# Kernel tuning notes

Measured on AMD Instinct MI355X. Metric: run time of the kernel, lower is better.

The kernel has to match this reference:

```python
import jax, jax.numpy as jnp
import numpy as np

B, CIN, COUT, H, W, KS, PAD = 8, 64, 128, 32, 32, 3, 1
OH, OW = H, W  # stride 1, pad 1, dilation 1 -> same spatial size
QMIN, QMAX = -128, 127


def setup_inputs() -> dict:
    key = jax.random.key(0)
    k1, k2, k3 = jax.random.split(key, 3)
    x = jax.random.normal(k1, (B, CIN, H, W), jnp.float32)
    weight = jax.random.normal(k2, (COUT, CIN, KS, KS), jnp.float32) * 0.05
    bias = jax.random.normal(k3, (COUT,), jnp.float32) * 0.01
    # exact int8 product LUT: lut[a+128, b+128] = a*b (the 'approximate multiplier' table)
    q = jnp.arange(QMIN, QMAX + 1, dtype=jnp.int32)  # [256]
    lut = q[:, None] * q[None, :]                     # [256,256] int32
    # gradient LUT: d(a*b)/da = b, d(a*b)/db = a
    gradient_lut = jnp.stack([
        jnp.broadcast_to(q[None, :], (256, 256)),
        jnp.broadcast_to(q[:, None], (256, 256)),
    ]).astype(jnp.float32)                            # [2,256,256]
    T_feature = jnp.ones((1,), jnp.float32)
    T_weight = jnp.ones((1,), jnp.float32)
    return {"x": x, "weight": weight, "bias": bias, "lut": lut,
            "gradient_lut": gradient_lut, "T_feature": T_feature, "T_weight": T_weight}


def _quantize(v, T):
    scale = 127.0 / T
    return jnp.clip(jnp.round(v * scale), QMIN, QMAX).astype(jnp.int32)


def _lut_conv(xq, wq, lut):
    """LUT-based int8 conv. xq [B,CIN,H,W] int32 in [-128,127], wq [COUT,CIN,KS,KS]."""
    xp = jnp.pad(xq, ((0, 0), (0, 0), (PAD, PAD), (PAD, PAD)))
    # im2col: 9 structurally-distinct kernel offsets (fixed small loop)
    patches = jnp.stack([xp[:, :, i:i + OH, j:j + OW]
                         for i in range(KS) for j in range(KS)], axis=2)  # [B,CIN,9,OH,OW]
    K = CIN * KS * KS
    cols = patches.transpose(0, 3, 4, 1, 2).reshape(B * OH * OW, K)  # [P,K]
    wf = wq.reshape(COUT, K)                                         # [COUT,K]
    lut_flat = lut.reshape(-1)

    def step(acc, xs):
        xk, wk = xs  # xk [P], wk [COUT]
        idx = (xk[:, None] + 128) * 256 + (wk[None, :] + 128)  # [P,COUT]
        return acc + lut_flat[idx], None

    acc0 = jnp.zeros((B * OH * OW, COUT), jnp.int32)
    acc, _ = jax.lax.scan(step, acc0, (cols.T, wf.T))  # scan over K patch elems
    return acc.reshape(B, OH, OW, COUT).transpose(0, 3, 1, 2)  # [B,COUT,OH,OW]


def reference(x, weight, bias, lut, gradient_lut, T_feature, T_weight):
    # EMA threshold update (update_T_func), detached scalars in the original
    Tf = 0.95 * T_feature[0] + 0.05 * jnp.max(jnp.abs(x))
    Tw = 0.95 * T_weight[0] + 0.05 * jnp.max(jnp.abs(weight))
    xq = _quantize(x, Tf)
    wq = _quantize(weight, Tw)
    acc = _lut_conv(xq, wq, lut).astype(jnp.float32)
    out = acc * ((Tf / 127.0) * (Tw / 127.0)) + bias[None, :, None, None]
    return out
```

## Files before the change

### kernel.cpp

```cpp
#include <hip/hip_runtime.h>
#include <cstdint>

#define BATCH 8
#define CIN 64
#define COUT 128
#define HH 32
#define WW 32

typedef int v4i __attribute__((ext_vector_type(4)));
typedef float v4f __attribute__((ext_vector_type(4)));

#define WS_TW 1
#define WS_PX 16
#define WFRAG_OFF 4096

#define TPITCH 18

__device__ __forceinline__ unsigned quantb(float v, float scale) {
    float q = rintf(v * scale);
    q = fminf(fmaxf(q, -128.0f), 127.0f);
    return ((unsigned)(int)q) & 255u;
}

__global__ __launch_bounds__(256) void prep(const float* __restrict__ x,
                                            const float* __restrict__ w,
                                            const float* __restrict__ Tw_in,
                                            float* __restrict__ ws_f32,
                                            uint8_t* __restrict__ wfrag) {
    int blk = blockIdx.x;
    int t = threadIdx.x;
    int lane = t & 63;
    int wave = t >> 6;
    __shared__ float sm[4];

    if (blk >= 18) {
        const float4* p = (const float4*)x;
        int xb = blk - 18;
        int base = xb * 1024 + t;
        float m = 0.0f;
        #pragma unroll
        for (int k = 0; k < 4; ++k) {
            float4 v = p[base + k * 256];
            m = fmaxf(m, fmaxf(fmaxf(fabsf(v.x), fabsf(v.y)), fmaxf(fabsf(v.z), fabsf(v.w))));
        }
        #pragma unroll
        for (int off = 32; off > 0; off >>= 1)
            m = fmaxf(m, __shfl_xor(m, off, 64));
        if (lane == 0) sm[wave] = m;
        __syncthreads();
        if (t == 0)
            ws_f32[WS_PX + xb] = fmaxf(fmaxf(sm[0], sm[1]), fmaxf(sm[2], sm[3]));
    } else {
        const float4* w4 = (const float4*)w;
        float m0 = 0.0f, m1 = 0.0f, m2 = 0.0f, m3 = 0.0f;
        #pragma unroll
        for (int i = 0; i < 72; i += 4) {
            float4 a = w4[t + (i + 0) * 256];
            float4 bv = w4[t + (i + 1) * 256];
            float4 c = w4[t + (i + 2) * 256];
            float4 d = w4[t + (i + 3) * 256];
            m0 = fmaxf(m0, fmaxf(fmaxf(fabsf(a.x), fabsf(a.y)), fmaxf(fabsf(a.z), fabsf(a.w))));
            m1 = fmaxf(m1, fmaxf(fmaxf(fabsf(bv.x), fabsf(bv.y)), fmaxf(fabsf(bv.z), fabsf(bv.w))));
            m2 = fmaxf(m2, fmaxf(fmaxf(fabsf(c.x), fabsf(c.y)), fmaxf(fabsf(c.z), fabsf(c.w))));
            m3 = fmaxf(m3, fmaxf(fmaxf(fabsf(d.x), fabsf(d.y)), fmaxf(fabsf(d.z), fabsf(d.w))));
        }
        float m = fmaxf(fmaxf(m0, m1), fmaxf(m2, m3));
        #pragma unroll
        for (int off = 32; off > 0; off >>= 1)
            m = fmaxf(m, __shfl_xor(m, off, 64));
        if (lane == 0) sm[wave] = m;
        __syncthreads();
        float Mw = fmaxf(fmaxf(sm[0], sm[1]), fmaxf(sm[2], sm[3]));
        float Tw = 0.95f * Tw_in[0] + 0.05f * Mw;
        if (blk == 0 && t == 0) ws_f32[WS_TW] = Tw;
        float scale = 127.0f / Tw;

        int wb = blk;
        #pragma unroll
        for (int k = 0; k < 4; ++k) {
            int d = wb * 1024 + k * 256 + t;
            int idx4 = d * 4;
            int j0 = idx4 & 15;
            int ln = (idx4 >> 4) & 63;
            int f  = idx4 >> 10;
            int g = f & 7;
            int tap = f >> 3;
            int kh = tap / 3, kw = tap - kh * 3;
            int co = g * 16 + (ln & 15);
            int ci0 = (ln >> 4) * 16 + j0;
            unsigned pack = 0;
            #pragma unroll
            for (int c = 0; c < 4; ++c) {
                float v = w[((co * CIN + ci0 + c) * 3 + kh) * 3 + kw];
                pack |= quantb(v, scale) << (8 * c);
            }
            ((unsigned*)wfrag)[d] = pack;
        }
    }
}

__global__ __launch_bounds__(256, 2) void conv_fused(const float* __restrict__ x,
                                                     const uint8_t* __restrict__ wfrag,
                                                     const float* __restrict__ bias,
                                                     const float* __restrict__ Tf_in,
                                                     const float* __restrict__ ws_f32,
                                                     float* __restrict__ out) {
    int blk = blockIdx.x;
    int t = threadIdx.x;
    int lane = t & 63;
    int wave = t >> 6;
    int nb = blk & 1;
    int mb = blk >> 1;
    int b = mb >> 5;
    int oh = mb & 31;

    __shared__ unsigned tile[3 * 34 * TPITCH];

    float p0 = ws_f32[WS_PX + lane];
    float p1 = ws_f32[WS_PX + 64 + lane];
    float Tw = ws_f32[WS_TW];

    if (t < 96) {
        int rr = t >> 5;
        int rest = t & 31;
        int side = rest >> 4;
        int kk = rest & 15;
        tile[(rr * 34 + side * 33) * TPITCH + kk] = 0u;
    }
    if (oh == 0 || oh == 31) {
        int rbad = (oh == 0) ? 0 : 2;
        #pragma unroll
        for (int k = 0; k < 3; ++k) {
            int i = t + k * 256;
            if (i < 544) {
                int px = i >> 4, kk = i & 15;
                tile[(rbad * 34 + px) * TPITCH + kk] = 0u;
            }
        }
    }

    float mx = fmaxf(p0, p1);
    #pragma unroll
    for (int off = 32; off > 0; off >>= 1)
        mx = fmaxf(mx, __shfl_xor(mx, off, 64));
    float Tf = 0.95f * Tf_in[0] + 0.05f * mx;
    float scale = 127.0f / Tf;

    const float4* x4 = (const float4*)x;
    #pragma unroll
    for (int k = 0; k < 2; ++k) {
        int j = t + k * 256;
        if (j < 384) {
            int r = j >> 7;
            int rem = j & 127;
            int wq = rem >> 4;
            int g4 = rem & 15;
            int ih = oh - 1 + r;
            if (ih >= 0 && ih < HH) {
                int xb = (b * CIN + g4 * 4) * 256 + ih * 8 + wq;
                float4 v0 = x4[xb];
                float4 v1 = x4[xb + 256];
                float4 v2 = x4[xb + 512];
                float4 v3 = x4[xb + 768];
                unsigned P0 = quantb(v0.x, scale) | (quantb(v0.y, scale) << 8) |
                              (quantb(v0.z, scale) << 16) | (quantb(v0.w, scale) << 24);
                unsigned P1 = quantb(v1.x, scale) | (quantb(v1.y, scale) << 8) |
                              (quantb(v1.z, scale) << 16) | (quantb(v1.w, scale) << 24);
                unsigned P2 = quantb(v2.x, scale) | (quantb(v2.y, scale) << 8) |
                              (quantb(v2.z, scale) << 16) | (quantb(v2.w, scale) << 24);
                unsigned P3 = quantb(v3.x, scale) | (quantb(v3.y, scale) << 8) |
                              (quantb(v3.z, scale) << 16) | (quantb(v3.w, scale) << 24);
                unsigned Q0 = __builtin_amdgcn_perm(P1, P0, 0x05040100u);
                unsigned Q1 = __builtin_amdgcn_perm(P1, P0, 0x07060302u);
                unsigned Q2 = __builtin_amdgcn_perm(P3, P2, 0x05040100u);
                unsigned Q3 = __builtin_amdgcn_perm(P3, P2, 0x07060302u);
                unsigned D0 = __builtin_amdgcn_perm(Q2, Q0, 0x06040200u);
                unsigned D1 = __builtin_amdgcn_perm(Q2, Q0, 0x07050301u);
                unsigned D2 = __builtin_amdgcn_perm(Q3, Q1, 0x06040200u);
                unsigned D3 = __builtin_amdgcn_perm(Q3, Q1, 0x07050301u);
                int base = (r * 34 + wq * 4 + 1) * TPITCH + g4;
                tile[base]              = D0;
                tile[base + TPITCH]     = D1;
                tile[base + 2 * TPITCH] = D2;
                tile[base + 3 * TPITCH] = D3;
            }
        }
    }
    __syncthreads();

    int mt = wave & 1;
    int nh2 = wave >> 1;
    int row = lane & 15;
    int quad = lane >> 4;
    int px0 = mt * 16 + row;

    v4i acc[2];
    acc[0] = (v4i){0, 0, 0, 0};
    acc[1] = (v4i){0, 0, 0, 0};

    const int2* tl2 = (const int2*)tile;

    #pragma unroll
    for (int tp = 0; tp < 9; ++tp) {
        const int kh = tp / 3, kw = tp % 3;
        int d = ((kh * 34) + px0 + kw) * TPITCH + quad * 4;
        int2 lo = tl2[(d >> 1)];
        int2 hi = tl2[(d >> 1) + 1];
        v4i afrag = (v4i){lo.x, lo.y, hi.x, hi.y};
        #pragma unroll
        for (int nt = 0; nt < 2; ++nt) {
            int g = nb * 4 + nh2 * 2 + nt;
            v4i bfrag = *(const v4i*)(wfrag + (((tp * 8 + g) * 64) + lane) * 16);
            acc[nt] = __builtin_amdgcn_mfma_i32_16x16x64_i8(afrag, bfrag, acc[nt], 0, 0, 0);
        }
    }

    float s = (Tf / 127.0f) * (Tw / 127.0f);
    int ow0 = mt * 16 + quad * 4;
    #pragma unroll
    for (int nt = 0; nt < 2; ++nt) {
        int g = nb * 4 + nh2 * 2 + nt;
        int co = g * 16 + row;
        float bb = bias[co];
        v4f o;
        o.x = (float)acc[nt][0] * s + bb;
        o.y = (float)acc[nt][1] * s + bb;
        o.z = (float)acc[nt][2] * s + bb;
        o.w = (float)acc[nt][3] * s + bb;
        __builtin_nontemporal_store(o, (v4f*)(out + (((b * COUT + co) * HH + oh) * WW) + ow0));
    }
}

extern "C" void kernel_launch(void* const* d_in, const int* in_sizes, int n_in,
                              void* d_out, int out_size, void* d_ws, size_t ws_size,
                              hipStream_t stream) {
    const float* x         = (const float*)d_in[0];
    const float* weight    = (const float*)d_in[1];
    const float* bias      = (const float*)d_in[2];
    const float* T_feature = (const float*)d_in[5];
    const float* T_weight  = (const float*)d_in[6];

    float*   ws_f32 = (float*)d_ws;
    uint8_t* wfrag  = (uint8_t*)d_ws + WFRAG_OFF;

    prep<<<146, 256, 0, stream>>>(x, weight, T_weight, ws_f32, wfrag);
    conv_fused<<<512, 256, 0, stream>>>(x, wfrag, bias, T_feature, ws_f32,
                                        (float*)d_out);
}
```

Baseline: 78.51 us.

## Fuse weight quantization into conv kernel, parallelize weight max reduction across blocks

The prep kernel no longer quantizes and repacks the weights into a global fragment buffer. It now only computes per-block partial abs-max values for x and w, with the weight reduction spread over 24 blocks instead of repeated in 18. Each conv block reduces both partials itself, derives Tw, and quantizes its own 64-channel half of the weights straight into a 36KB LDS fragment buffer. This removes the serial per-block full-weight scan and one global round-trip, but every one of the 512 blocks now redoes weight loading and quantization, and the extra LDS may lower occupancy.

After: 78.95 us. About the same (+0.6%).

```diff
diff --git a/kernel.cpp b/kernel.cpp
--- a/kernel.cpp
+++ b/kernel.cpp
@@ -10,9 +10,8 @@
 typedef int v4i __attribute__((ext_vector_type(4)));
 typedef float v4f __attribute__((ext_vector_type(4)));
 
-#define WS_TW 1
 #define WS_PX 16
-#define WFRAG_OFF 4096
+#define WS_PW 160
 
 #define TPITCH 18
 
@@ -22,87 +21,50 @@
     return ((unsigned)(int)q) & 255u;
 }
 
-__global__ __launch_bounds__(256) void prep(const float* __restrict__ x,
-                                            const float* __restrict__ w,
-                                            const float* __restrict__ Tw_in,
-                                            float* __restrict__ ws_f32,
-                                            uint8_t* __restrict__ wfrag) {
+__global__ __launch_bounds__(256) void partials(const float* __restrict__ x,
+                                                const float* __restrict__ w,
+                                                float* __restrict__ ws_f32) {
     int blk = blockIdx.x;
     int t = threadIdx.x;
     int lane = t & 63;
     int wave = t >> 6;
     __shared__ float sm[4];
 
-    if (blk >= 18) {
+    float m = 0.0f;
+    if (blk < 128) {
         const float4* p = (const float4*)x;
-        int xb = blk - 18;
-        int base = xb * 1024 + t;
-        float m = 0.0f;
+        int base = blk * 1024 + t;
         #pragma unroll
         for (int k = 0; k < 4; ++k) {
             float4 v = p[base + k * 256];
             m = fmaxf(m, fmaxf(fmaxf(fabsf(v.x), fabsf(v.y)), fmaxf(fabsf(v.z), fabsf(v.w))));
         }
-        #pragma unroll
-        for (int off = 32; off > 0; off >>= 1)
-            m = fmaxf(m, __shfl_xor(m, off, 64));
-        if (lane == 0) sm[wave] = m;
-        __syncthreads();
-        if (t == 0)
-            ws_f32[WS_PX + xb] = fmaxf(fmaxf(sm[0], sm[1]), fmaxf(sm[2], sm[3]));
     } else {
-        const float4* w4 = (const float4*)w;
-        float m0 = 0.0f, m1 = 0.0f, m2 = 0.0f, m3 = 0.0f;
-        #pragma unroll
-        for (int i = 0; i < 72; i += 4) {
-            float4 a = w4[t + (i + 0) * 256];
-            float4 bv = w4[t + (i + 1) * 256];
-            float4 c = w4[t + (i + 2) * 256];
-            float4 d = w4[t + (i + 3) * 256];
-            m0 = fmaxf(m0, fmaxf(fmaxf(fabsf(a.x), fabsf(a.y)), fmaxf(fabsf(a.z), fabsf(a.w))));
-            m1 = fmaxf(m1, fmaxf(fmaxf(fabsf(bv.x), fabsf(bv.y)), fmaxf(fabsf(bv.z), fabsf(bv.w))));
-            m2 = fmaxf(m2, fmaxf(fmaxf(fabsf(c.x), fabsf(c.y)), fmaxf(fabsf(c.z), fabsf(c.w))));
-            m3 = fmaxf(m3, fmaxf(fmaxf(fabsf(d.x), fabsf(d.y)), fmaxf(fabsf(d.z), fabsf(d.w))));
-        }
-        float m = fmaxf(fmaxf(m0, m1), fmaxf(m2, m3));
-        #pragma unroll
-        for (int off = 32; off > 0; off >>= 1)
-            m = fmaxf(m, __shfl_xor(m, off, 64));
-        if (lane == 0) sm[wave] = m;
-        __syncthreads();
-        float Mw = fmaxf(fmaxf(sm[0], sm[1]), fmaxf(sm[2], sm[3]));
-        float Tw = 0.95f * Tw_in[0] + 0.05f * Mw;
-        if (blk == 0 && t == 0) ws_f32[WS_TW] = Tw;
-        float scale = 127.0f / Tw;
-
-        int wb = blk;
-        #pragma unroll
-        for (int k = 0; k < 4; ++k) {
-            int d = wb * 1024 + k * 256 + t;
-            int idx4 = d * 4;
-            int j0 = idx4 & 15;
-            int ln = (idx4 >> 4) & 63;
-            int f  = idx4 >> 10;
-            int g = f & 7;
-            int tap = f >> 3;
-            int kh = tap / 3, kw = tap - kh * 3;
-            int co = g * 16 + (ln & 15);
-            int ci0 = (ln >> 4) * 16 + j0;
-            unsigned pack = 0;
-            #pragma unroll
-            for (int c = 0; c < 4; ++c) {
-                float v = w[((co * CIN + ci0 + c) * 3 + kh) * 3 + kw];
-                pack |= quantb(v, scale) << (8 * c);
-            }
-            ((unsigned*)wfrag)[d] = pack;
-        }
+        const float4* p = (const float4*)w;
+        int base = (blk - 128) * 768 + t;
+        #pragma unroll
+        for (int k = 0; k < 3; ++k) {
+            float4 v = p[base + k * 256];
+            m = fmaxf(m, fmaxf(fmaxf(fabsf(v.x), fabsf(v.y)), fmaxf(fabsf(v.z), fabsf(v.w))));
+        }
+    }
+    #pragma unroll
+    for (int off = 32; off > 0; off >>= 1)
+        m = fmaxf(m, __shfl_xor(m, off, 64));
+    if (lane == 0) sm[wave] = m;
+    __syncthreads();
+    if (t == 0) {
+        float r = fmaxf(fmaxf(sm[0], sm[1]), fmaxf(sm[2], sm[3]));
+        if (blk < 128) ws_f32[WS_PX + blk] = r;
+        else           ws_f32[WS_PW + (blk - 128)] = r;
     }
 }
 
 __global__ __launch_bounds__(256, 2) void conv_fused(const float* __restrict__ x,
-                                                     const uint8_t* __restrict__ wfrag,
+                                                     const float* __restrict__ w,
                                                      const float* __restrict__ bias,
                                                      const float* __restrict__ Tf_in,
+                                                     const float* __restrict__ Tw_in,
                                                      const float* __restrict__ ws_f32,
                                                      float* __restrict__ out) {
     int blk = blockIdx.x;
@@ -115,10 +77,21 @@
     int oh = mb & 31;
 
     __shared__ unsigned tile[3 * 34 * TPITCH];
+    __shared__ unsigned bfrag[9 * 4 * 64 * 4];
 
     float p0 = ws_f32[WS_PX + lane];
     float p1 = ws_f32[WS_PX + 64 + lane];
-    float Tw = ws_f32[WS_TW];
+    float pw = ws_f32[WS_PW + (lane < 24 ? lane : 0)];
+    float mx = fmaxf(p0, p1);
+    #pragma unroll
+    for (int off = 32; off > 0; off >>= 1) {
+        mx = fmaxf(mx, __shfl_xor(mx, off, 64));
+        pw = fmaxf(pw, __shfl_xor(pw, off, 64));
+    }
+    float Tf = 0.95f * Tf_in[0] + 0.05f * mx;
+    float Tw = 0.95f * Tw_in[0] + 0.05f * pw;
+    float scf = 127.0f / Tf;
+    float scw = 127.0f / Tw;
 
     if (t < 96) {
         int rr = t >> 5;
@@ -139,12 +112,39 @@
         }
     }
 
-    float mx = fmaxf(p0, p1);
-    #pragma unroll
-    for (int off = 32; off > 0; off >>= 1)
-        mx = fmaxf(mx, __shfl_xor(mx, off, 64));
-    float Tf = 0.95f * Tf_in[0] + 0.05f * mx;
-    float scale = 127.0f / Tf;
+    {
+        int co0 = nb * 64;
+        int ln = t >> 2;
+        int j0g = t & 3;
+        const float4* w4 = (const float4*)w;
+        #pragma unroll
+        for (int gl = 0; gl < 4; ++gl) {
+            int co = co0 + gl * 16 + (ln & 15);
+            int ci0 = (ln >> 4) * 16 + j0g * 4;
+            int F0 = co * 576 + ci0 * 9;
+            float4 r0 = w4[(F0 >> 2) + 0];
+            float4 r1 = w4[(F0 >> 2) + 1];
+            float4 r2 = w4[(F0 >> 2) + 2];
+            float4 r3 = w4[(F0 >> 2) + 3];
+            float4 r4 = w4[(F0 >> 2) + 4];
+            float4 r5 = w4[(F0 >> 2) + 5];
+            float4 r6 = w4[(F0 >> 2) + 6];
+            float4 r7 = w4[(F0 >> 2) + 7];
+            float4 r8 = w4[(F0 >> 2) + 8];
+            float fl[36];
+            *(float4*)&fl[0]  = r0; *(float4*)&fl[4]  = r1; *(float4*)&fl[8]  = r2;
+            *(float4*)&fl[12] = r3; *(float4*)&fl[16] = r4; *(float4*)&fl[20] = r5;
+            *(float4*)&fl[24] = r6; *(float4*)&fl[28] = r7; *(float4*)&fl[32] = r8;
+            #pragma unroll
+            for (int tap = 0; tap < 9; ++tap) {
+                unsigned pk = quantb(fl[tap], scw)
+                            | (quantb(fl[9 + tap], scw) << 8)
+                            | (quantb(fl[18 + tap], scw) << 16)
+                            | (quantb(fl[27 + tap], scw) << 24);
+                bfrag[tap * 1024 + gl * 256 + t] = pk;
+            }
+        }
+    }
 
     const float4* x4 = (const float4*)x;
     #pragma unroll
@@ -162,14 +162,14 @@
                 float4 v1 = x4[xb + 256];
                 float4 v2 = x4[xb + 512];
                 float4 v3 = x4[xb + 768];
-                unsigned P0 = quantb(v0.x, scale) | (quantb(v0.y, scale) << 8) |
-                              (quantb(v0.z, scale) << 16) | (quantb(v0.w, scale) << 24);
-                unsigned P1 = quantb(v1.x, scale) | (quantb(v1.y, scale) << 8) |
-                              (quantb(v1.z, scale) << 16) | (quantb(v1.w, scale) << 24);
-                unsigned P2 = quantb(v2.x, scale) | (quantb(v2.y, scale) << 8) |
-                              (quantb(v2.z, scale) << 16) | (quantb(v2.w, scale) << 24);
-                unsigned P3 = quantb(v3.x, scale) | (quantb(v3.y, scale) << 8) |
-                              (quantb(v3.z, scale) << 16) | (quantb(v3.w, scale) << 24);
+                unsigned P0 = quantb(v0.x, scf) | (quantb(v0.y, scf) << 8) |
+                              (quantb(v0.z, scf) << 16) | (quantb(v0.w, scf) << 24);
+                unsigned P1 = quantb(v1.x, scf) | (quantb(v1.y, scf) << 8) |
+                              (quantb(v1.z, scf) << 16) | (quantb(v1.w, scf) << 24);
+                unsigned P2 = quantb(v2.x, scf) | (quantb(v2.y, scf) << 8) |
+                              (quantb(v2.z, scf) << 16) | (quantb(v2.w, scf) << 24);
+                unsigned P3 = quantb(v3.x, scf) | (quantb(v3.y, scf) << 8) |
+                              (quantb(v3.z, scf) << 16) | (quantb(v3.w, scf) << 24);
                 unsigned Q0 = __builtin_amdgcn_perm(P1, P0, 0x05040100u);
                 unsigned Q1 = __builtin_amdgcn_perm(P1, P0, 0x07060302u);
                 unsigned Q2 = __builtin_amdgcn_perm(P3, P2, 0x05040100u);
@@ -199,6 +199,7 @@
     acc[1] = (v4i){0, 0, 0, 0};
 
     const int2* tl2 = (const int2*)tile;
+    const v4i* bf4 = (const v4i*)bfrag;
 
     #pragma unroll
     for (int tp = 0; tp < 9; ++tp) {
@@ -209,9 +210,9 @@
         v4i afrag = (v4i){lo.x, lo.y, hi.x, hi.y};
         #pragma unroll
         for (int nt = 0; nt < 2; ++nt) {
-            int g = nb * 4 + nh2 * 2 + nt;
-            v4i bfrag = *(const v4i*)(wfrag + (((tp * 8 + g) * 64) + lane) * 16);
-            acc[nt] = __builtin_amdgcn_mfma_i32_16x16x64_i8(afrag, bfrag, acc[nt], 0, 0, 0);
+            int gl = nh2 * 2 + nt;
+            v4i bv = bf4[(tp * 4 + gl) * 64 + lane];
+            acc[nt] = __builtin_amdgcn_mfma_i32_16x16x64_i8(afrag, bv, acc[nt], 0, 0, 0);
         }
     }
 
@@ -219,8 +220,8 @@
     int ow0 = mt * 16 + quad * 4;
     #pragma unroll
     for (int nt = 0; nt < 2; ++nt) {
-        int g = nb * 4 + nh2 * 2 + nt;
-        int co = g * 16 + row;
+        int gl = nh2 * 2 + nt;
+        int co = nb * 64 + gl * 16 + row;
         float bb = bias[co];
         v4f o;
         o.x = (float)acc[nt][0] * s + bb;
@@ -240,10 +241,9 @@
     const float* T_feature = (const float*)d_in[5];
     const float* T_weight  = (const float*)d_in[6];
 
-    float*   ws_f32 = (float*)d_ws;
-    uint8_t* wfrag  = (uint8_t*)d_ws + WFRAG_OFF;
-
-    prep<<<146, 256, 0, stream>>>(x, weight, T_weight, ws_f32, wfrag);
-    conv_fused<<<512, 256, 0, stream>>>(x, wfrag, bias, T_feature, ws_f32,
-                                        (float*)d_out);
-}
+    float* ws_f32 = (float*)d_ws;
+
+    partials<<<152, 256, 0, stream>>>(x, weight, ws_f32);
+    conv_fused<<<512, 256, 0, stream>>>(x, weight, bias, T_feature, T_weight,
+                                        ws_f32, (float*)d_out);
+}
```
